# Kernel optimization log

Hardware: AMD Instinct MI355X
Metric: run time of the kernel (lower is better)

Reference implementation:

```python
import jax, jax.numpy as jnp
import numpy as np

N = 100000   # nodes
E = 1600000  # edges (avg degree 16)
D = 128      # in_features == out_features
THETA = 0.25  # hardcoded in the original forward (overwrites log(lamda/l+1))


def setup_inputs() -> dict:
    key = jax.random.key(0)
    k0, k1, k2, k3, k4, k5, k6 = jax.random.split(key, 7)
    stdv = 1.0 / np.sqrt(D)
    return {
        "input": jax.random.normal(k0, (N, D), dtype=jnp.float32),
        "edge_src": jax.random.randint(k1, (E,), 0, N),
        "edge_dst": jax.random.randint(k2, (E,), 0, N),
        "edge_val": jax.random.uniform(k3, (E,), dtype=jnp.float32),
        "h0": jax.random.normal(k4, (N, D), dtype=jnp.float32),
        "weight": jax.random.uniform(k5, (D, D), dtype=jnp.float32, minval=-stdv, maxval=stdv),
        "alpha": jnp.full((1,), 0.4, dtype=jnp.float32),
        "lamda": 1,
        "l": 4,
    }


def reference(input, edge_src, edge_dst, edge_val, h0, weight, alpha, lamda, l):
    # hi = spmm(adj, input): gather source node features, scale by edge weight,
    # segment-sum into destination rows.  [E, D] intermediate -> [N, D]
    hi = jax.ops.segment_sum(input[edge_src] * edge_val[:, None], edge_dst, num_segments=N)
    # original uses alpha.data (detached): sigmoid(alpha)/2
    a = jax.lax.stop_gradient(jax.nn.sigmoid(alpha) / 2.0)  # [1], broadcasts
    # variant=False: support == r == alpha-blend of aggregated and initial features
    support = (1.0 - a) * hi + a * h0
    # theta-scaled dense matmul epilogue + identity-mapping blend
    output = THETA * (support @ weight) + (1.0 - THETA) * support
    # residual=True
    return output + input
```

## Files before the change

### kernel.cpp

```cpp
#include <hip/hip_runtime.h>
#include <hip/hip_bf16.h>

#define DFEAT 128
#define THETA 0.25f
#define SRC_MASK 0xFFFFF
#define DLOW_SH 20
#define SLOWF (1 << 30)
#define SCAP 6144

typedef __attribute__((ext_vector_type(8))) short short8;
typedef __attribute__((ext_vector_type(4))) float f32x4;
typedef __attribute__((ext_vector_type(2))) int i32x2;

__device__ inline unsigned short bf16_bits(float x) {
    __hip_bfloat16 h = __float2bfloat16(x);
    return *reinterpret_cast<unsigned short*>(&h);
}
__device__ inline unsigned pk_bf16(float x, float y) {
    return (unsigned)bf16_bits(x) | ((unsigned)bf16_bits(y) << 16);
}
__device__ inline void fma8(float* A, const uint4 x, float v) {
    A[0] = fmaf(v, __uint_as_float(x.x << 16),         A[0]);
    A[1] = fmaf(v, __uint_as_float(x.x & 0xffff0000u), A[1]);
    A[2] = fmaf(v, __uint_as_float(x.y << 16),         A[2]);
    A[3] = fmaf(v, __uint_as_float(x.y & 0xffff0000u), A[3]);
    A[4] = fmaf(v, __uint_as_float(x.z << 16),         A[4]);
    A[5] = fmaf(v, __uint_as_float(x.z & 0xffff0000u), A[5]);
    A[6] = fmaf(v, __uint_as_float(x.w << 16),         A[6]);
    A[7] = fmaf(v, __uint_as_float(x.w & 0xffff0000u), A[7]);
}

__global__ __launch_bounds__(256) void k_cvt(const float* __restrict__ in,
                                             uint4* __restrict__ o, int n8,
                                             int* __restrict__ bcnt) {
    if (blockIdx.x == 0) {
        bcnt[threadIdx.x] = 0;
        bcnt[threadIdx.x + 256] = 0;
    }
    int i = blockIdx.x * blockDim.x + threadIdx.x;
    if (i >= n8) return;
    float4 a = reinterpret_cast<const float4*>(in)[(size_t)i * 2];
    float4 b = reinterpret_cast<const float4*>(in)[(size_t)i * 2 + 1];
    uint4 r;
    r.x = pk_bf16(a.x, a.y);
    r.y = pk_bf16(a.z, a.w);
    r.z = pk_bf16(b.x, b.y);
    r.w = pk_bf16(b.z, b.w);
    o[i] = r;
}

__global__ __launch_bounds__(512) void k_bhist(const int* __restrict__ edst,
                                               int* __restrict__ bcnt, int E) {
    __shared__ int h[512];
    int t = threadIdx.x;
    h[t] = 0;
    __syncthreads();
    int e0 = blockIdx.x * 4096;
    #pragma unroll
    for (int k = 0; k < 8; ++k) {
        int e = e0 + t + k * 512;
        if (e < E) atomicAdd(&h[edst[e] >> 8], 1);
    }
    __syncthreads();
    if (h[t]) atomicAdd(&bcnt[t], h[t]);
}

__global__ __launch_bounds__(512) void k_bscan_wprep(
    const int* __restrict__ bcnt, int* __restrict__ bbase,
    int* __restrict__ tail, int* __restrict__ rowptr,
    int NBUCK, int N, int E,
    const float* __restrict__ W, unsigned short* __restrict__ wp)
{
    if (blockIdx.x == 0) {
        __shared__ int buf[512];
        int t = threadIdx.x;
        buf[t] = (t < NBUCK) ? bcnt[t] : 0;
        __syncthreads();
        for (int off = 1; off < 512; off <<= 1) {
            int y = (t >= off) ? buf[t - off] : 0;
            __syncthreads();
            buf[t] += y;
            __syncthreads();
        }
        if (t < NBUCK) {
            int base = t ? buf[t - 1] : 0;
            bbase[t] = base;
            tail[t]  = base;
        }
        if (t == 0) { bbase[NBUCK] = E; rowptr[N] = E; }
    } else {
        int item = (blockIdx.x - 1) * 512 + threadIdx.x;
        if (item >= 16 * DFEAT) return;
        int kg = item >> 7;
        int n  = item & 127;
        unsigned pk4[4];
        #pragma unroll
        for (int jj = 0; jj < 4; ++jj) {
            int k0 = kg * 8 + jj * 2;
            float w0 = THETA * W[(size_t)k0 * DFEAT + n];
            float w1 = THETA * W[(size_t)(k0 + 1) * DFEAT + n];
            if (k0 == n)     w0 += 1.0f - THETA;
            if (k0 + 1 == n) w1 += 1.0f - THETA;
            pk4[jj] = pk_bf16(w0, w1);
        }
        uint4 v = make_uint4(pk4[0], pk4[1], pk4[2], pk4[3]);
        int slot = kg ^ (n & 7);
        *reinterpret_cast<uint4*>(&wp[n * DFEAT + slot * 8]) = v;
    }
}

__global__ __launch_bounds__(512) void k_bpart(
    const int* __restrict__ esrc, const int* __restrict__ edst,
    const float* __restrict__ eval_, int* __restrict__ tail,
    int2* __restrict__ csr, int E)
{
    __shared__ int histB[512];
    __shared__ int offsB[512];
    __shared__ int gbase[512];
    __shared__ unsigned short bkOf[4096];
    __shared__ int2 stage[4096];

    int t  = threadIdx.x;
    int e0 = blockIdx.x * 4096;
    int szb = min(4096, E - e0);

    histB[t] = 0;
    __syncthreads();

    int myb[8], myr[8];
    int2 mye[8];
    #pragma unroll
    for (int k = 0; k < 8; ++k) {
        int e = e0 + t + k * 512;
        myb[k] = -1;
        if (e < E) {
            int d = edst[e];
            int b = d >> 8;
            mye[k] = make_int2(esrc[e] | ((d & 255) << DLOW_SH),
                               __float_as_int(eval_[e]));
            myb[k] = b;
            myr[k] = atomicAdd(&histB[b], 1);
        }
    }
    __syncthreads();

    offsB[t] = histB[t];
    __syncthreads();
    for (int off = 1; off < 512; off <<= 1) {
        int y = (t >= off) ? offsB[t - off] : 0;
        __syncthreads();
        offsB[t] += y;
        __syncthreads();
    }
    if (histB[t] > 0) gbase[t] = atomicAdd(&tail[t], histB[t]);
    __syncthreads();

    #pragma unroll
    for (int k = 0; k < 8; ++k) {
        if (myb[k] >= 0) {
            int exb = myb[k] ? offsB[myb[k] - 1] : 0;
            int x = exb + myr[k];
            stage[x] = mye[k];
            bkOf[x]  = (unsigned short)myb[k];
        }
    }
    __syncthreads();

    for (int j = t; j < szb; j += 512) {
        int b   = bkOf[j];
        int exb = b ? offsB[b - 1] : 0;
        csr[gbase[b] + (j - exb)] = stage[j];
    }
}

__global__ __launch_bounds__(512) void k_bsort(const int* __restrict__ bbase,
                                               int2* __restrict__ csr,
                                               int* __restrict__ rowptr, int N)
{
    __shared__ int2 stage[SCAP];
    __shared__ int cntN[256];
    __shared__ int offsN[256];
    __shared__ int curN[256];

    int b  = blockIdx.x;
    int lo = bbase[b], hi = bbase[b + 1];
    int sz = hi - lo;
    int t  = threadIdx.x;
    int node0 = b << 8;

    if (sz > SCAP) {
        if (t < 256) { int n = node0 + t; if (n < N) rowptr[n] = lo | SLOWF; }
        return;
    }

    if (t < 256) cntN[t] = 0;
    for (int j = t; j < sz; j += 512) stage[j] = csr[lo + j];
    __syncthreads();
    for (int j = t; j < sz; j += 512)
        atomicAdd(&cntN[(stage[j].x >> DLOW_SH) & 255], 1);
    __syncthreads();

    if (t < 256) offsN[t] = cntN[t];
    __syncthreads();
    for (int off = 1; off < 256; off <<= 1) {
        int y = (t >= off && t < 256) ? offsN[t - off] : 0;
        __syncthreads();
        if (t < 256) offsN[t] += y;
        __syncthreads();
    }
    if (t < 256) {
        int ex = t ? offsN[t - 1] : 0;
        curN[t] = ex;
        int n = node0 + t;
        if (n < N) rowptr[n] = lo + ex;
    }
    __syncthreads();

    for (int j = t; j < sz; j += 512) {
        int n = (stage[j].x >> DLOW_SH) & 255;
        int pos = atomicAdd(&curN[n], 1);
        csr[lo + pos] = stage[j];
    }
}

__global__ __launch_bounds__(256) void k_fused5(
    const unsigned short* __restrict__ in16, const int2* __restrict__ csr,
    const int* __restrict__ rowptr, const float* __restrict__ h0,
    const float* __restrict__ input, const unsigned short* __restrict__ wp,
    const float* __restrict__ alpha, float* __restrict__ out, int N)
{
    __shared__ unsigned short At[16 * DFEAT];

    const int wv   = threadIdx.x >> 6;
    const int lane = threadIdx.x & 63;
    const int ng   = lane >> 4;
    const int s    = lane & 15;

    const int row0 = blockIdx.x * 16;
    const int r    = wv * 4 + ng;
    const int node = row0 + r;

    const float a   = 0.5f / (1.0f + __expf(-alpha[0]));
    const float oma = 1.0f - a;

    float A[8] = {0.f, 0.f, 0.f, 0.f, 0.f, 0.f, 0.f, 0.f};

    if (node < N) {
        int rp = rowptr[node];
        int beg, end;
        if (rp & SLOWF) {
            beg = rp & ~SLOWF;
            int nn = min((((node >> 8) + 1) << 8), N);
            end = rowptr[nn] & ~SLOWF;
        } else {
            beg = rp;
            end = rowptr[node + 1] & ~SLOWF;
        }
        const int dlow = node & 255;

        for (int e = beg; e < end; e += 16) {
            i32x2 p[16];
            uint4 x[16];
            float v[16];
            #pragma unroll
            for (int i = 0; i < 16; ++i) {
                int idx = (e + i < end) ? (e + i) : beg;
                p[i] = __builtin_nontemporal_load(
                    reinterpret_cast<const i32x2*>(&csr[idx]));
            }
            #pragma unroll
            for (int i = 0; i < 16; ++i) {
                x[i] = *reinterpret_cast<const uint4*>(
                    &in16[(size_t)(p[i].x & SRC_MASK) * DFEAT + s * 8]);
                bool ok = (e + i < end) && (((p[i].x >> DLOW_SH) & 255) == dlow);
                v[i] = ok ? __int_as_float(p[i].y) : 0.f;
            }
            #pragma unroll
            for (int i = 0; i < 16; ++i) fma8(A, x[i], v[i]);
        }

        size_t gb = (size_t)node * DFEAT + s * 8;
        f32x4 h0a = __builtin_nontemporal_load(
            reinterpret_cast<const f32x4*>(&h0[gb]));
        f32x4 h0b = __builtin_nontemporal_load(
            reinterpret_cast<const f32x4*>(&h0[gb + 4]));
        float b0 = oma * A[0] + a * h0a.x;
        float b1 = oma * A[1] + a * h0a.y;
        float b2 = oma * A[2] + a * h0a.z;
        float b3 = oma * A[3] + a * h0a.w;
        float b4 = oma * A[4] + a * h0b.x;
        float b5 = oma * A[5] + a * h0b.y;
        float b6 = oma * A[6] + a * h0b.z;
        float b7 = oma * A[7] + a * h0b.w;
        uint4 pk;
        pk.x = pk_bf16(b0, b1);
        pk.y = pk_bf16(b2, b3);
        pk.z = pk_bf16(b4, b5);
        pk.w = pk_bf16(b6, b7);
        *reinterpret_cast<uint4*>(&At[r * DFEAT + ((s ^ (r & 7)) << 3)]) = pk;
    }
    __syncthreads();

    const int m  = lane & 15;
    const int kb = lane >> 4;
    const int n1 = wv * 32 + m;
    const int n2 = n1 + 16;

    short8 bw1[4], bw2[4];
    #pragma unroll
    for (int kk = 0; kk < 4; ++kk) {
        int w = kk * 4 + kb;
        bw1[kk] = *reinterpret_cast<const short8*>(
            &wp[n1 * DFEAT + ((w ^ (n1 & 7)) << 3)]);
        bw2[kk] = *reinterpret_cast<const short8*>(
            &wp[n2 * DFEAT + ((w ^ (n2 & 7)) << 3)]);
    }

    f32x4 acc0 = {0.f, 0.f, 0.f, 0.f};
    f32x4 acc1 = {0.f, 0.f, 0.f, 0.f};
    #pragma unroll
    for (int kk = 0; kk < 4; ++kk) {
        short8 af = *reinterpret_cast<const short8*>(
            &At[m * DFEAT + (((kk * 4 + kb) ^ (m & 7)) << 3)]);
        acc0 = __builtin_amdgcn_mfma_f32_16x16x32_bf16(af, bw1[kk], acc0, 0, 0, 0);
        acc1 = __builtin_amdgcn_mfma_f32_16x16x32_bf16(af, bw2[kk], acc1, 0, 0, 0);
    }

    #pragma unroll
    for (int q = 0; q < 4; ++q) {
        int row = row0 + kb * 4 + q;
        if (row < N) {
            size_t gi = (size_t)row * DFEAT + n1;
            float r0 = __builtin_nontemporal_load(&input[gi]);
            float r1 = __builtin_nontemporal_load(&input[gi + 16]);
            __builtin_nontemporal_store(acc0[q] + r0, &out[gi]);
            __builtin_nontemporal_store(acc1[q] + r1, &out[gi + 16]);
        }
    }
}

__global__ void k_hist(const int* __restrict__ edst, int* __restrict__ cnt, int E) {
    int i = blockIdx.x * blockDim.x + threadIdx.x;
    int e4 = i * 4;
    if (e4 + 4 <= E) {
        int4 d = *reinterpret_cast<const int4*>(&edst[e4]);
        atomicAdd(&cnt[d.x], 1);
        atomicAdd(&cnt[d.y], 1);
        atomicAdd(&cnt[d.z], 1);
        atomicAdd(&cnt[d.w], 1);
    } else {
        for (int e = e4; e < E; ++e) atomicAdd(&cnt[edst[e]], 1);
    }
}

__global__ void k_scanA(const int* __restrict__ cnt, int* __restrict__ part, int N) {
    __shared__ int s[256];
    int i = blockIdx.x * 256 + threadIdx.x;
    s[threadIdx.x] = (i < N) ? cnt[i] : 0;
    __syncthreads();
    for (int off = 128; off > 0; off >>= 1) {
        if (threadIdx.x < off) s[threadIdx.x] += s[threadIdx.x + off];
        __syncthreads();
    }
    if (threadIdx.x == 0) part[blockIdx.x] = s[0];
}

__global__ void k_scanB(int* __restrict__ part, int* __restrict__ rowptr, int B, int N) {
    __shared__ int buf[1024];
    int t = threadIdx.x;
    buf[t] = (t < B) ? part[t] : 0;
    __syncthreads();
    for (int off = 1; off < 1024; off <<= 1) {
        int y = (t >= off) ? buf[t - off] : 0;
        __syncthreads();
        buf[t] += y;
        __syncthreads();
    }
    if (t < B) part[t] = (t == 0) ? 0 : buf[t - 1];
    if (t == B - 1) rowptr[N] = buf[t];
}

__global__ void k_scanC(const int* __restrict__ cnt, const int* __restrict__ part,
                        int* __restrict__ rowptr, int N) {
    __shared__ int buf[256];
    int t = threadIdx.x;
    int i = blockIdx.x * 256 + t;
    buf[t] = (i < N) ? cnt[i] : 0;
    __syncthreads();
    for (int off = 1; off < 256; off <<= 1) {
        int y = (t >= off) ? buf[t - off] : 0;
        __syncthreads();
        buf[t] += y;
        __syncthreads();
    }
    if (i < N) rowptr[i] = part[blockIdx.x] + ((t == 0) ? 0 : buf[t - 1]);
}

__global__ void k_slot(const int* __restrict__ esrc, const int* __restrict__ edst,
                       const float* __restrict__ eval_, const int* __restrict__ rowptr,
                       int* __restrict__ cnt, int2* __restrict__ csr, int E) {
    int i = blockIdx.x * blockDim.x + threadIdx.x;
    int e4 = i * 4;
    if (e4 + 4 <= E) {
        int4   s = *reinterpret_cast<const int4*>(&esrc[e4]);
        int4   d = *reinterpret_cast<const int4*>(&edst[e4]);
        float4 v = *reinterpret_cast<const float4*>(&eval_[e4]);
        int r;
        r = atomicSub(&cnt[d.x], 1); csr[rowptr[d.x] + r - 1] = make_int2(s.x, __float_as_int(v.x));
        r = atomicSub(&cnt[d.y], 1); csr[rowptr[d.y] + r - 1] = make_int2(s.y, __float_as_int(v.y));
        r = atomicSub(&cnt[d.z], 1); csr[rowptr[d.z] + r - 1] = make_int2(s.z, __float_as_int(v.z));
        r = atomicSub(&cnt[d.w], 1); csr[rowptr[d.w] + r - 1] = make_int2(s.w, __float_as_int(v.w));
    } else {
        for (int e = e4; e < E; ++e) {
            int d = edst[e];
            int r = atomicSub(&cnt[d], 1);
            csr[rowptr[d] + r - 1] = make_int2(esrc[e], __float_as_int(eval_[e]));
        }
    }
}

__global__ __launch_bounds__(256) void k_gather(
    const float* __restrict__ input, const int2* __restrict__ csr,
    const int* __restrict__ rowptr, const float* __restrict__ h0,
    const float* __restrict__ alpha, float* __restrict__ out, int N)
{
    int w    = (int)(((long long)blockIdx.x * blockDim.x + threadIdx.x) >> 6);
    int lane = threadIdx.x & 63;
    if (w >= N) return;
    int beg = rowptr[w], end = rowptr[w + 1];
    float ax = 0.f, ay = 0.f, bx = 0.f, by = 0.f;
    int i = beg;
    for (; i + 2 <= end; i += 2) {
        int2 p0 = csr[i], p1 = csr[i + 1];
        float2 x0 = *(const float2*)&input[(size_t)p0.x * DFEAT + lane * 2];
        float2 x1 = *(const float2*)&input[(size_t)p1.x * DFEAT + lane * 2];
        float v0 = __int_as_float(p0.y), v1 = __int_as_float(p1.y);
        ax = fmaf(v0, x0.x, ax); ay = fmaf(v0, x0.y, ay);
        bx = fmaf(v1, x1.x, bx); by = fmaf(v1, x1.y, by);
    }
    if (i < end) {
        int2 p = csr[i];
        float2 x = *(const float2*)&input[(size_t)p.x * DFEAT + lane * 2];
        float v = __int_as_float(p.y);
        ax = fmaf(v, x.x, ax); ay = fmaf(v, x.y, ay);
    }
    float hx = ax + bx, hy = ay + by;
    float a   = 0.5f / (1.0f + __expf(-alpha[0]));
    float oma = 1.0f - a;
    float2 h0v = *(const float2*)&h0[(size_t)w * DFEAT + lane * 2];
    float2 sv;
    sv.x = oma * hx + a * h0v.x;
    sv.y = oma * hy + a * h0v.y;
    *(float2*)&out[(size_t)w * DFEAT + lane * 2] = sv;
}

__global__ __launch_bounds__(256) void gcn_scatter(
    const float* __restrict__ input, const int* __restrict__ esrc,
    const int* __restrict__ edst, const float* __restrict__ eval_,
    float* __restrict__ hi, int E)
{
    long long t = (long long)blockIdx.x * blockDim.x + threadIdx.x;
    int e = (int)(t >> 6);
    if (e >= E) return;
    int lane = (int)(t & 63);
    int s = esrc[e]; int d = edst[e]; float v = eval_[e];
    const float2 x = *reinterpret_cast<const float2*>(&input[(size_t)s * DFEAT + lane * 2]);
    float* p = &hi[(size_t)d * DFEAT + lane * 2];
    unsafeAtomicAdd(p,     x.x * v);
    unsafeAtomicAdd(p + 1, x.y * v);
}

template <bool BLEND>
__global__ __launch_bounds__(256) void gcn_epilogue(
    float* __restrict__ out, const float* __restrict__ h0,
    const float* __restrict__ inp, const float* __restrict__ W,
    const float* __restrict__ alpha, int N)
{
    __shared__ __hip_bfloat16 Wl[DFEAT * DFEAT];
    __shared__ float4 S4[16][DFEAT / 4];

    const float a   = 0.5f / (1.0f + __expf(-alpha[0]));
    const float oma = 1.0f - a;

    for (int i = threadIdx.x; i < DFEAT * DFEAT; i += 256) {
        int k = i >> 7, j = i & 127;
        float w = W[i] * THETA;
        if (k == j) w += 1.0f - THETA;
        Wl[i] = __float2bfloat16(w);
    }

    const int j  = threadIdx.x & 127;
    const int rg = threadIdx.x >> 7;

    for (int base = blockIdx.x * 16; base < N; base += gridDim.x * 16) {
        const int rows = min(16, N - base);
        __syncthreads();
        for (int i = threadIdx.x; i < rows * 32; i += 256) {
            int r = i >> 5, c = i & 31;
            size_t gph = (size_t)(base + r) * (DFEAT / 4) + c;
            float4 hv = reinterpret_cast<const float4*>(out)[gph];
            float4 sv;
            if (BLEND) {
                float4 h0v = reinterpret_cast<const float4*>(h0)[gph];
                sv.x = oma * hv.x + a * h0v.x;
                sv.y = oma * hv.y + a * h0v.y;
                sv.z = oma * hv.z + a * h0v.z;
                sv.w = oma * hv.w + a * h0v.w;
            } else {
                sv = hv;
            }
            S4[r][c] = sv;
        }
        __syncthreads();

        float acc[8];
        #pragma unroll
        for (int r = 0; r < 8; r++) acc[r] = 0.0f;
        for (int k = 0; k < DFEAT; k += 4) {
            float w0 = __bfloat162float(Wl[(k + 0) * DFEAT + j]);
            float w1 = __bfloat162float(Wl[(k + 1) * DFEAT + j]);
            float w2 = __bfloat162float(Wl[(k + 2) * DFEAT + j]);
            float w3 = __bfloat162float(Wl[(k + 3) * DFEAT + j]);
            #pragma unroll
            for (int r = 0; r < 8; r++) {
                float4 s4 = S4[rg * 8 + r][k >> 2];
                acc[r] = fmaf(s4.x, w0, acc[r]);
                acc[r] = fmaf(s4.y, w1, acc[r]);
                acc[r] = fmaf(s4.z, w2, acc[r]);
                acc[r] = fmaf(s4.w, w3, acc[r]);
            }
        }
        #pragma unroll
        for (int r = 0; r < 8; r++) {
            int rr = rg * 8 + r;
            if (rr < rows) {
                size_t gph = (size_t)(base + rr) * DFEAT + j;
                out[gph] = acc[r] + inp[gph];
            }
        }
    }
}

extern "C" void kernel_launch(void* const* d_in, const int* in_sizes, int n_in,
                              void* d_out, int out_size, void* d_ws, size_t ws_size,
                              hipStream_t stream) {
    const float* input = (const float*)d_in[0];
    const int*   esrc  = (const int*)  d_in[1];
    const int*   edst  = (const int*)  d_in[2];
    const float* eval_ = (const float*)d_in[3];
    const float* h0    = (const float*)d_in[4];
    const float* W     = (const float*)d_in[5];
    const float* alpha = (const float*)d_in[6];

    const int N = in_sizes[0] / DFEAT;
    const int E = in_sizes[1];
    float* out = (float*)d_out;
    const int B = (N + 255) / 256;

    size_t bA_in16   = 0;
    size_t bA_csr    = (bA_in16 + (size_t)N * DFEAT * 2 + 15) & ~(size_t)15;
    size_t bA_rowptr = bA_csr + (size_t)E * 8;
    size_t bA_bkt    = bA_rowptr + (size_t)(N + 1) * 4;
    size_t bA_wp     = (bA_bkt + (size_t)N * 4 + 15) & ~(size_t)15;
    size_t needA     = bA_wp + (size_t)DFEAT * DFEAT * 2;

    size_t o_rowptr = 0;
    size_t o_cnt    = o_rowptr + (size_t)(N + 1);
    size_t o_part   = o_cnt + (size_t)N;
    size_t o_csr    = (o_part + 1024 + 1) & ~(size_t)1;
    size_t needB    = o_csr * 4 + (size_t)E * 8;

    const int NBUCK = (N + 255) >> 8;

    if (ws_size >= needA && N <= 131072 && N >= 1600) {
        unsigned short* in16 = (unsigned short*)((char*)d_ws + bA_in16);
        int2* csr    = (int2*)((char*)d_ws + bA_csr);
        int*  rowptr = (int*) ((char*)d_ws + bA_rowptr);
        int*  bcnt   = (int*) ((char*)d_ws + bA_bkt);
        int*  bbase  = bcnt + 512;
        int*  tail   = bbase + 513;
        unsigned short* wp = (unsigned short*)((char*)d_ws + bA_wp);

        int n8     = N * DFEAT / 8;
        int ntiles = (N + 15) / 16;
        int nEB    = (E + 4095) / 4096;

        k_cvt  <<<dim3((n8 + 255) / 256), dim3(256), 0, stream>>>(input, (uint4*)in16,
                                                                  n8, bcnt);
        k_bhist<<<dim3(nEB),              dim3(512), 0, stream>>>(edst, bcnt, E);
        k_bscan_wprep<<<dim3(5),          dim3(512), 0, stream>>>(bcnt, bbase, tail,
                                                                  rowptr, NBUCK, N, E,
                                                                  W, wp);
        k_bpart<<<dim3(nEB),              dim3(512), 0, stream>>>(esrc, edst, eval_,
                                                                  tail, csr, E);
        k_bsort<<<dim3(NBUCK),            dim3(512), 0, stream>>>(bbase, csr, rowptr, N);
        k_fused5<<<dim3(ntiles),          dim3(256), 0, stream>>>(in16, csr, rowptr,
                                                                  h0, input, wp, alpha,
                                                                  out, N);
    } else if (ws_size >= needB && B <= 1024) {
        int*  rowptr = (int*)d_ws + o_rowptr;
        int*  cnt    = (int*)d_ws + o_cnt;
        int*  part   = (int*)d_ws + o_part;
        int2* csr    = (int2*)((int*)d_ws + o_csr);
        int E4 = (E + 3) / 4;

        hipMemsetAsync(cnt, 0, (size_t)N * sizeof(int), stream);
        k_hist <<<dim3((E4 + 255) / 256), dim3(256), 0, stream>>>(edst, cnt, E);
        k_scanA<<<dim3(B),               dim3(256), 0, stream>>>(cnt, part, N);
        k_scanB<<<dim3(1),               dim3(1024), 0, stream>>>(part, rowptr, B, N);
        k_scanC<<<dim3(B),               dim3(256), 0, stream>>>(cnt, part, rowptr, N);
        k_slot <<<dim3((E4 + 255) / 256), dim3(256), 0, stream>>>(esrc, edst, eval_,
                                                                  rowptr, cnt, csr, E);
        k_gather<<<dim3((N + 3) / 4),    dim3(256), 0, stream>>>(input, csr, rowptr,
                                                                 h0, alpha, out, N);
        gcn_epilogue<false><<<dim3(2048), dim3(256), 0, stream>>>(out, h0, input, W,
                                                                  alpha, N);
    } else {
        hipMemsetAsync(out, 0, (size_t)N * DFEAT * sizeof(float), stream);
        long long threads = (long long)E * 64;
        unsigned  nblk    = (unsigned)((threads + 255) / 256);
        gcn_scatter<<<dim3(nblk), dim3(256), 0, stream>>>(input, esrc, edst, eval_, out, E);
        gcn_epilogue<true><<<dim3(2048), dim3(256), 0, stream>>>(out, h0, input, W,
                                                                 alpha, N);
    }
}
```

Before: 171.8 us.

## Merge convert and histogram kernels; process 64 rows per fused SpMM-GEMM block

Combines the bf16 conversion and the bucket histogram into one launch split by block index, and clears the bucket counters with a memset instead of inside the convert kernel. The fused gather/GEMM kernel now handles 64 rows per block: each 16-lane group gathers four nodes one after another with an unroll of 8, and the weight fragments loaded into registers are reused across four MFMA row tiles. This cuts per-block weight loads and launch overhead. The cost is fewer blocks, fewer outstanding gathers per thread and serialized node processing, which could lower latency hiding in the memory-bound gather.

```diff
diff --git a/kernel.cpp b/kernel.cpp
--- a/kernel.cpp
+++ b/kernel.cpp
@@ -30,39 +30,35 @@
     A[7] = fmaf(v, __uint_as_float(x.w & 0xffff0000u), A[7]);
 }
 
-__global__ __launch_bounds__(256) void k_cvt(const float* __restrict__ in,
-                                             uint4* __restrict__ o, int n8,
-                                             int* __restrict__ bcnt) {
-    if (blockIdx.x == 0) {
-        bcnt[threadIdx.x] = 0;
-        bcnt[threadIdx.x + 256] = 0;
-    }
-    int i = blockIdx.x * blockDim.x + threadIdx.x;
-    if (i >= n8) return;
-    float4 a = reinterpret_cast<const float4*>(in)[(size_t)i * 2];
-    float4 b = reinterpret_cast<const float4*>(in)[(size_t)i * 2 + 1];
-    uint4 r;
-    r.x = pk_bf16(a.x, a.y);
-    r.y = pk_bf16(a.z, a.w);
-    r.z = pk_bf16(b.x, b.y);
-    r.w = pk_bf16(b.z, b.w);
-    o[i] = r;
-}
-
-__global__ __launch_bounds__(512) void k_bhist(const int* __restrict__ edst,
-                                               int* __restrict__ bcnt, int E) {
-    __shared__ int h[512];
+__global__ __launch_bounds__(512) void k_cvt_hist(
+    const float* __restrict__ in, uint4* __restrict__ o, int n8, int cvtB,
+    const int* __restrict__ edst, int* __restrict__ bcnt, int E)
+{
     int t = threadIdx.x;
-    h[t] = 0;
-    __syncthreads();
-    int e0 = blockIdx.x * 4096;
-    #pragma unroll
-    for (int k = 0; k < 8; ++k) {
-        int e = e0 + t + k * 512;
-        if (e < E) atomicAdd(&h[edst[e] >> 8], 1);
-    }
-    __syncthreads();
-    if (h[t]) atomicAdd(&bcnt[t], h[t]);
+    if ((int)blockIdx.x < cvtB) {
+        int i = blockIdx.x * 512 + t;
+        if (i >= n8) return;
+        float4 a = reinterpret_cast<const float4*>(in)[(size_t)i * 2];
+        float4 b = reinterpret_cast<const float4*>(in)[(size_t)i * 2 + 1];
+        uint4 r;
+        r.x = pk_bf16(a.x, a.y);
+        r.y = pk_bf16(a.z, a.w);
+        r.z = pk_bf16(b.x, b.y);
+        r.w = pk_bf16(b.z, b.w);
+        o[i] = r;
+    } else {
+        __shared__ int h[512];
+        h[t] = 0;
+        __syncthreads();
+        int e0 = (blockIdx.x - cvtB) * 4096;
+        #pragma unroll
+        for (int k = 0; k < 8; ++k) {
+            int e = e0 + t + k * 512;
+            if (e < E) atomicAdd(&h[edst[e] >> 8], 1);
+        }
+        __syncthreads();
+        if (h[t]) atomicAdd(&bcnt[t], h[t]);
+    }
 }
 
 __global__ __launch_bounds__(512) void k_bscan_wprep(
@@ -223,81 +219,85 @@
     }
 }
 
-__global__ __launch_bounds__(256) void k_fused5(
+__global__ __launch_bounds__(256) void k_fused6(
     const unsigned short* __restrict__ in16, const int2* __restrict__ csr,
     const int* __restrict__ rowptr, const float* __restrict__ h0,
     const float* __restrict__ input, const unsigned short* __restrict__ wp,
     const float* __restrict__ alpha, float* __restrict__ out, int N)
 {
-    __shared__ unsigned short At[16 * DFEAT];
+    __shared__ unsigned short At[64 * DFEAT];
 
     const int wv   = threadIdx.x >> 6;
     const int lane = threadIdx.x & 63;
     const int ng   = lane >> 4;
     const int s    = lane & 15;
-
-    const int row0 = blockIdx.x * 16;
-    const int r    = wv * 4 + ng;
-    const int node = row0 + r;
+    const int G    = wv * 4 + ng;
+
+    const int row0 = blockIdx.x * 64;
 
     const float a   = 0.5f / (1.0f + __expf(-alpha[0]));
     const float oma = 1.0f - a;
 
-    float A[8] = {0.f, 0.f, 0.f, 0.f, 0.f, 0.f, 0.f, 0.f};
-
-    if (node < N) {
-        int rp = rowptr[node];
-        int beg, end;
-        if (rp & SLOWF) {
-            beg = rp & ~SLOWF;
-            int nn = min((((node >> 8) + 1) << 8), N);
-            end = rowptr[nn] & ~SLOWF;
-        } else {
-            beg = rp;
-            end = rowptr[node + 1] & ~SLOWF;
-        }
-        const int dlow = node & 255;
-
-        for (int e = beg; e < end; e += 16) {
-            i32x2 p[16];
-            uint4 x[16];
-            float v[16];
-            #pragma unroll
-            for (int i = 0; i < 16; ++i) {
-                int idx = (e + i < end) ? (e + i) : beg;
-                p[i] = __builtin_nontemporal_load(
-                    reinterpret_cast<const i32x2*>(&csr[idx]));
+    #pragma unroll 1
+    for (int j = 0; j < 4; ++j) {
+        const int r    = G * 4 + j;
+        const int node = row0 + r;
+        float A[8] = {0.f, 0.f, 0.f, 0.f, 0.f, 0.f, 0.f, 0.f};
+        if (node < N) {
+            int rp = rowptr[node];
+            int beg, end;
+            if (rp & SLOWF) {
+                beg = rp & ~SLOWF;
+                int nn = min((((node >> 8) + 1) << 8), N);
+                end = rowptr[nn] & ~SLOWF;
+            } else {
+                beg = rp;
+                end = rowptr[node + 1] & ~SLOWF;
             }
-            #pragma unroll
-            for (int i = 0; i < 16; ++i) {
-                x[i] = *reinterpret_cast<const uint4*>(
-                    &in16[(size_t)(p[i].x & SRC_MASK) * DFEAT + s * 8]);
-                bool ok = (e + i < end) && (((p[i].x >> DLOW_SH) & 255) == dlow);
-                v[i] = ok ? __int_as_float(p[i].y) : 0.f;
+            const int dlow = node & 255;
+
+            for (int e = beg; e < end; e += 8) {
+                i32x2 p[8];
+                uint4 x[8];
+                float v[8];
+                #pragma unroll
+                for (int i = 0; i < 8; ++i) {
+                    int idx = (e + i < end) ? (e + i) : beg;
+                    p[i] = __builtin_nontemporal_load(
+                        reinterpret_cast<const i32x2*>(&csr[idx]));
+                }
+                #pragma unroll
+                for (int i = 0; i < 8; ++i) {
+                    x[i] = *reinterpret_cast<const uint4*>(
+                        &in16[(size_t)(p[i].x & SRC_MASK) * DFEAT + s * 8]);
+                    bool ok = (e + i < end) &&
+                              (((p[i].x >> DLOW_SH) & 255) == dlow);
+                    v[i] = ok ? __int_as_float(p[i].y) : 0.f;
+                }
+                #pragma unroll
+                for (int i = 0; i < 8; ++i) fma8(A, x[i], v[i]);
             }
-            #pragma unroll
-            for (int i = 0; i < 16; ++i) fma8(A, x[i], v[i]);
-        }
-
-        size_t gb = (size_t)node * DFEAT + s * 8;
-        f32x4 h0a = __builtin_nontemporal_load(
-            reinterpret_cast<const f32x4*>(&h0[gb]));
-        f32x4 h0b = __builtin_nontemporal_load(
-            reinterpret_cast<const f32x4*>(&h0[gb + 4]));
-        float b0 = oma * A[0] + a * h0a.x;
-        float b1 = oma * A[1] + a * h0a.y;
-        float b2 = oma * A[2] + a * h0a.z;
-        float b3 = oma * A[3] + a * h0a.w;
-        float b4 = oma * A[4] + a * h0b.x;
-        float b5 = oma * A[5] + a * h0b.y;
-        float b6 = oma * A[6] + a * h0b.z;
-        float b7 = oma * A[7] + a * h0b.w;
-        uint4 pk;
-        pk.x = pk_bf16(b0, b1);
-        pk.y = pk_bf16(b2, b3);
-        pk.z = pk_bf16(b4, b5);
-        pk.w = pk_bf16(b6, b7);
-        *reinterpret_cast<uint4*>(&At[r * DFEAT + ((s ^ (r & 7)) << 3)]) = pk;
+
+            size_t gb = (size_t)node * DFEAT + s * 8;
+            f32x4 h0a = __builtin_nontemporal_load(
+                reinterpret_cast<const f32x4*>(&h0[gb]));
+            f32x4 h0b = __builtin_nontemporal_load(
+                reinterpret_cast<const f32x4*>(&h0[gb + 4]));
+            float b0 = oma * A[0] + a * h0a.x;
+            float b1 = oma * A[1] + a * h0a.y;
+            float b2 = oma * A[2] + a * h0a.z;
+            float b3 = oma * A[3] + a * h0a.w;
+            float b4 = oma * A[4] + a * h0b.x;
+            float b5 = oma * A[5] + a * h0b.y;
+            float b6 = oma * A[6] + a * h0b.z;
+            float b7 = oma * A[7] + a * h0b.w;
+            uint4 pk;
+            pk.x = pk_bf16(b0, b1);
+            pk.y = pk_bf16(b2, b3);
+            pk.z = pk_bf16(b4, b5);
+            pk.w = pk_bf16(b6, b7);
+            *reinterpret_cast<uint4*>(&At[r * DFEAT + ((s ^ (r & 7)) << 3)]) = pk;
+        }
     }
     __syncthreads();
 
@@ -316,25 +316,27 @@
             &wp[n2 * DFEAT + ((w ^ (n2 & 7)) << 3)]);
     }
 
-    f32x4 acc0 = {0.f, 0.f, 0.f, 0.f};
-    f32x4 acc1 = {0.f, 0.f, 0.f, 0.f};
     #pragma unroll
-    for (int kk = 0; kk < 4; ++kk) {
-        short8 af = *reinterpret_cast<const short8*>(
-            &At[m * DFEAT + (((kk * 4 + kb) ^ (m & 7)) << 3)]);
-        acc0 = __builtin_amdgcn_mfma_f32_16x16x32_bf16(af, bw1[kk], acc0, 0, 0, 0);
-        acc1 = __builtin_amdgcn_mfma_f32_16x16x32_bf16(af, bw2[kk], acc1, 0, 0, 0);
-    }
-
-    #pragma unroll
-    for (int q = 0; q < 4; ++q) {
-        int row = row0 + kb * 4 + q;
-        if (row < N) {
-            size_t gi = (size_t)row * DFEAT + n1;
-            float r0 = __builtin_nontemporal_load(&input[gi]);
-            float r1 = __builtin_nontemporal_load(&input[gi + 16]);
-            __builtin_nontemporal_store(acc0[q] + r0, &out[gi]);
-            __builtin_nontemporal_store(acc1[q] + r1, &out[gi + 16]);
+    for (int rb = 0; rb < 4; ++rb) {
+        f32x4 acc0 = {0.f, 0.f, 0.f, 0.f};
+        f32x4 acc1 = {0.f, 0.f, 0.f, 0.f};
+        #pragma unroll
+        for (int kk = 0; kk < 4; ++kk) {
+            short8 af = *reinterpret_cast<const short8*>(
+                &At[(rb * 16 + m) * DFEAT + (((kk * 4 + kb) ^ (m & 7)) << 3)]);
+            acc0 = __builtin_amdgcn_mfma_f32_16x16x32_bf16(af, bw1[kk], acc0, 0, 0, 0);
+            acc1 = __builtin_amdgcn_mfma_f32_16x16x32_bf16(af, bw2[kk], acc1, 0, 0, 0);
+        }
+        #pragma unroll
+        for (int q = 0; q < 4; ++q) {
+            int row = row0 + rb * 16 + kb * 4 + q;
+            if (row < N) {
+                size_t gi = (size_t)row * DFEAT + n1;
+                float r0 = __builtin_nontemporal_load(&input[gi]);
+                float r1 = __builtin_nontemporal_load(&input[gi + 16]);
+                __builtin_nontemporal_store(acc0[q] + r0, &out[gi]);
+                __builtin_nontemporal_store(acc1[q] + r1, &out[gi + 16]);
+            }
         }
     }
 }
@@ -582,21 +584,22 @@
         unsigned short* wp = (unsigned short*)((char*)d_ws + bA_wp);
 
         int n8     = N * DFEAT / 8;
-        int ntiles = (N + 15) / 16;
+        int ntiles = (N + 63) / 64;
         int nEB    = (E + 4095) / 4096;
-
-        k_cvt  <<<dim3((n8 + 255) / 256), dim3(256), 0, stream>>>(input, (uint4*)in16,
-                                                                  n8, bcnt);
-        k_bhist<<<dim3(nEB),              dim3(512), 0, stream>>>(edst, bcnt, E);
-        k_bscan_wprep<<<dim3(5),          dim3(512), 0, stream>>>(bcnt, bbase, tail,
-                                                                  rowptr, NBUCK, N, E,
-                                                                  W, wp);
-        k_bpart<<<dim3(nEB),              dim3(512), 0, stream>>>(esrc, edst, eval_,
-                                                                  tail, csr, E);
-        k_bsort<<<dim3(NBUCK),            dim3(512), 0, stream>>>(bbase, csr, rowptr, N);
-        k_fused5<<<dim3(ntiles),          dim3(256), 0, stream>>>(in16, csr, rowptr,
-                                                                  h0, input, wp, alpha,
-                                                                  out, N);
+        int cvtB   = (n8 + 511) / 512;
+
+        hipMemsetAsync(bcnt, 0, 512 * sizeof(int), stream);
+        k_cvt_hist<<<dim3(cvtB + nEB),   dim3(512), 0, stream>>>(input, (uint4*)in16,
+                                                                 n8, cvtB, edst, bcnt, E);
+        k_bscan_wprep<<<dim3(5),         dim3(512), 0, stream>>>(bcnt, bbase, tail,
+                                                                 rowptr, NBUCK, N, E,
+                                                                 W, wp);
+        k_bpart<<<dim3(nEB),             dim3(512), 0, stream>>>(esrc, edst, eval_,
+                                                                 tail, csr, E);
+        k_bsort<<<dim3(NBUCK),           dim3(512), 0, stream>>>(bbase, csr, rowptr, N);
+        k_fused6<<<dim3(ntiles),         dim3(256), 0, stream>>>(in16, csr, rowptr,
+                                                                 h0, input, wp, alpha,
+                                                                 out, N);
     } else if (ws_size >= needB && B <= 1024) {
         int*  rowptr = (int*)d_ws + o_rowptr;
         int*  cnt    = (int*)d_ws + o_cnt;
```

Result: no change. 172.6 us (+0.5%).
